# Optimization experiments

Hardware: AMD Instinct MI355X
Metric: run time of the kernel (lower is better)

The kernel has to match this reference:

```python
import jax, jax.numpy as jnp
import numpy as np
import math

B, T, D, H = 2, 2048, 1024, 16
HD = D // H  # head_dim = 64
DFF = 4 * D
EPS = 1e-5


def gelu_tanh(x):
    c = math.sqrt(2.0 / math.pi)
    return 0.5 * x * (1.0 + jnp.tanh(c * (x + 0.044715 * x ** 3)))


def layernorm(x, scale, shift):
    mean = jnp.mean(x, axis=-1, keepdims=True)
    var = jnp.mean((x - mean) ** 2, axis=-1, keepdims=True)
    return scale * (x - mean) / jnp.sqrt(var + EPS) + shift


def setup_inputs() -> dict:
    key = jax.random.key(0)
    ks = jax.random.split(key, 10)
    s_in = 1.0 / math.sqrt(D)
    s_ff = 1.0 / math.sqrt(DFF)
    return {
        "x": jax.random.normal(ks[0], (B, T, D), dtype=jnp.float32),
        "Wq": jax.random.normal(ks[1], (D, D), dtype=jnp.float32) * s_in,
        "Wk": jax.random.normal(ks[2], (D, D), dtype=jnp.float32) * s_in,
        "Wv": jax.random.normal(ks[3], (D, D), dtype=jnp.float32) * s_in,
        "Wo": jax.random.normal(ks[4], (D, D), dtype=jnp.float32) * s_in,
        "bo": jnp.zeros((D,), dtype=jnp.float32),
        "W1": jax.random.normal(ks[5], (D, DFF), dtype=jnp.float32) * s_in,
        "b1": jnp.zeros((DFF,), dtype=jnp.float32),
        "W2": jax.random.normal(ks[6], (DFF, D), dtype=jnp.float32) * s_ff,
        "b2": jnp.zeros((D,), dtype=jnp.float32),
        "g1": jnp.ones((D,), dtype=jnp.float32),
        "s1": jnp.zeros((D,), dtype=jnp.float32),
        "g2": jnp.ones((D,), dtype=jnp.float32),
        "s2": jnp.zeros((D,), dtype=jnp.float32),
    }


def reference(x, Wq, Wk, Wv, Wo, bo, W1, b1, W2, b2, g1, s1, g2, s2):
    # --- attention sublayer (pre-LN) ---
    h = layernorm(x, g1, s1)
    q = (h @ Wq).reshape(B, T, H, HD).transpose(0, 2, 1, 3)  # [B,H,T,hd]
    k = (h @ Wk).reshape(B, T, H, HD).transpose(0, 2, 1, 3)
    v = (h @ Wv).reshape(B, T, H, HD).transpose(0, 2, 1, 3)
    scores = jnp.einsum('bhqd,bhkd->bhqk', q, k) / math.sqrt(HD)
    causal = jnp.triu(jnp.ones((T, T), dtype=bool), k=1)
    scores = jnp.where(causal, -jnp.inf, scores)
    attn = jax.nn.softmax(scores, axis=-1)
    ctx = jnp.einsum('bhqk,bhkd->bhqd', attn, v)
    ctx = ctx.transpose(0, 2, 1, 3).reshape(B, T, D)
    x = x + (ctx @ Wo + bo)
    # --- feed-forward sublayer (pre-LN) ---
    h2 = layernorm(x, g2, s2)
    ff = gelu_tanh(h2 @ W1 + b1) @ W2 + b2
    return x + ff
```

## Files before the change

### kernel.cpp

```cpp
#include <hip/hip_runtime.h>
#include <cstdint>
#include <cstddef>

typedef unsigned short u16;
typedef __attribute__((ext_vector_type(8))) __bf16 bf16x8;
typedef __attribute__((ext_vector_type(8))) unsigned short u16x8;
typedef __attribute__((ext_vector_type(4))) float f32x4;
typedef __attribute__((ext_vector_type(16))) float f32x16;
typedef __attribute__((ext_vector_type(4))) unsigned short u16x4;
typedef __attribute__((ext_vector_type(2))) int i32x2;

#define DEV __device__ __forceinline__

DEV u16 f2bf(float f) {
  union { float f; unsigned u; } v; v.f = f;
  unsigned r = v.u + 0x7fffu + ((v.u >> 16) & 1u);
  return (u16)(r >> 16);
}

DEV float bf2f(u16 b) {
  unsigned u = ((unsigned)b) << 16;
  union { unsigned u; float f; } v; v.u = u;
  return v.f;
}

DEV void gload_lds16(const void* g, void* l) {
  __builtin_amdgcn_global_load_lds(
      (const __attribute__((address_space(1))) void*)g,
      (__attribute__((address_space(3))) void*)l, 16, 0, 0);
}

DEV float gelu_f(float x) {
  float u = 0.7978845608028654f * (x + 0.044715f * x * x * x);
  float t = exp2f(-2.8853900817779268f * u);
  return x * __builtin_amdgcn_rcpf(1.0f + t);
}

DEV unsigned cvtpk_bf16(float lo, float hi) {
  unsigned u;
  asm("v_cvt_pk_bf16_f32 %0, %1, %2" : "=v"(u) : "v"(lo), "v"(hi));
  return u;
}

__global__ __launch_bounds__(256) void wtrans(const float* __restrict__ W,
                                              u16* __restrict__ Wt, int K, int N) {
  __shared__ float tile[32][33];
  const int n0 = blockIdx.x * 32, k0 = blockIdx.y * 32;
  const int t = threadIdx.x, c = t & 31, r0 = t >> 5;
#pragma unroll
  for (int i = 0; i < 4; ++i) {
    int r = r0 + i * 8;
    tile[r][c] = W[(size_t)(k0 + r) * N + n0 + c];
  }
  __syncthreads();
#pragma unroll
  for (int i = 0; i < 4; ++i) {
    int r = r0 + i * 8;
    Wt[(size_t)(n0 + r) * K + k0 + c] = f2bf(tile[c][r]);
  }
}

__global__ __launch_bounds__(256) void ln_bf16(const float* __restrict__ x,
                                               const float* __restrict__ g,
                                               const float* __restrict__ s,
                                               u16* __restrict__ out) {
  const int row = blockIdx.x, t = threadIdx.x;
  const int l = t & 63, w = t >> 6;
  f32x4 v = *(const f32x4*)(x + (size_t)row * 1024 + t * 4);
  float sm = v.x + v.y + v.z + v.w;
  float s2 = v.x * v.x + v.y * v.y + v.z * v.z + v.w * v.w;
#pragma unroll
  for (int d = 1; d < 64; d <<= 1) { sm += __shfl_xor(sm, d); s2 += __shfl_xor(s2, d); }
  __shared__ float red[8];
  if (l == 0) { red[w] = sm; red[4 + w] = s2; }
  __syncthreads();
  sm = red[0] + red[1] + red[2] + red[3];
  s2 = red[4] + red[5] + red[6] + red[7];
  const float mean = sm * (1.0f / 1024.0f);
  const float rstd = rsqrtf(s2 * (1.0f / 1024.0f) - mean * mean + 1e-5f);
  f32x4 gv = *(const f32x4*)(g + t * 4);
  f32x4 sv = *(const f32x4*)(s + t * 4);
  u16x4 o;
  o.x = f2bf((v.x - mean) * rstd * gv.x + sv.x);
  o.y = f2bf((v.y - mean) * rstd * gv.y + sv.y);
  o.z = f2bf((v.z - mean) * rstd * gv.z + sv.z);
  o.w = f2bf((v.w - mean) * rstd * gv.w + sv.w);
  *(u16x4*)(out + (size_t)row * 1024 + t * 4) = o;
}

template <int EPI>
__global__ __launch_bounds__(256) void gemm_bt(const u16* __restrict__ A,
                                               const u16* __restrict__ Bt,
                                               const float* __restrict__ bias,
                                               const float* __restrict__ resid,
                                               void* __restrict__ outp,
                                               void* __restrict__ outpB,
                                               void* __restrict__ outpC,
                                               void* __restrict__ outpD,
                                               int M, int N, int K) {
  __shared__ alignas(16) u16 As[128 * 32];
  __shared__ alignas(16) u16 Bs[128 * 32];
  const int tid = threadIdx.x, l = tid & 63, w = tid >> 6;
  const int bm0 = blockIdx.x * 128, bn0 = blockIdx.y * 128;
  const int wm = (w >> 1) * 64, wn = (w & 1) * 64;
  const int lr = l & 15, lk8 = (l >> 4) * 8;

  const int z = blockIdx.z;
  const int Kc = K / gridDim.z;
  const int kbeg = z * Kc, kend = kbeg + Kc;
  void* po = outp;
  if (EPI == 3) po = (z == 0) ? outp : (z == 1) ? outpB : (z == 2) ? outpC : outpD;

  f32x4 acc[4][4];
#pragma unroll
  for (int i = 0; i < 4; ++i)
#pragma unroll
    for (int j = 0; j < 4; ++j) acc[i][j] = (f32x4){0.f, 0.f, 0.f, 0.f};

  for (int k0 = kbeg; k0 < kend; k0 += 32) {
#pragma unroll
    for (int c = 0; c < 2; ++c) {
      const int lin = c * 256 + tid;
      const int row = lin >> 2, col = (lin & 3) * 8;
      gload_lds16(A + (size_t)(bm0 + row) * K + k0 + col, (char*)As + lin * 16);
      gload_lds16(Bt + (size_t)(bn0 + row) * K + k0 + col, (char*)Bs + lin * 16);
    }
    __syncthreads();
    bf16x8 af[4], bfv[4];
#pragma unroll
    for (int i = 0; i < 4; ++i) af[i] = *(const bf16x8*)(As + (wm + i * 16 + lr) * 32 + lk8);
#pragma unroll
    for (int j = 0; j < 4; ++j) bfv[j] = *(const bf16x8*)(Bs + (wn + j * 16 + lr) * 32 + lk8);
#pragma unroll
    for (int i = 0; i < 4; ++i)
#pragma unroll
      for (int j = 0; j < 4; ++j)
        acc[i][j] = __builtin_amdgcn_mfma_f32_16x16x32_bf16(af[i], bfv[j], acc[i][j], 0, 0, 0);
    __syncthreads();
  }

#pragma unroll
  for (int i = 0; i < 4; ++i) {
#pragma unroll
    for (int r = 0; r < 4; ++r) {
      const int m = bm0 + wm + i * 16 + (l >> 4) * 4 + r;
#pragma unroll
      for (int j = 0; j < 4; ++j) {
        const int n = bn0 + wn + j * 16 + lr;
        const float va = acc[i][j][r];
        if (EPI == 0) {
          ((u16*)po)[(size_t)m * N + n] = f2bf(va);
        } else if (EPI == 1) {
          ((u16*)po)[(size_t)m * N + n] = f2bf(gelu_f(va + bias[n]));
        } else if (EPI == 2) {
          ((float*)po)[(size_t)m * N + n] = va + bias[n] + resid[(size_t)m * N + n];
        } else {
          ((u16*)po)[(size_t)m * N + n] = f2bf(va);
        }
      }
    }
  }
}

__global__ __launch_bounds__(256) void reduce4(const u16* __restrict__ p0,
                                               const u16* __restrict__ p1,
                                               const u16* __restrict__ p2,
                                               const u16* __restrict__ p3,
                                               const float* __restrict__ bias,
                                               const float* __restrict__ resid,
                                               float* __restrict__ out) {
  const int m = blockIdx.x, t = threadIdx.x;
  const size_t off = (size_t)m * 1024 + t * 4;
  const u16x4 a0 = *(const u16x4*)(p0 + off);
  const u16x4 a1 = *(const u16x4*)(p1 + off);
  const u16x4 a2 = *(const u16x4*)(p2 + off);
  const u16x4 a3 = *(const u16x4*)(p3 + off);
  const f32x4 rv = *(const f32x4*)(resid + off);
  const f32x4 bv = *(const f32x4*)(bias + t * 4);
  f32x4 o;
  o.x = bf2f(a0.x) + bf2f(a1.x) + bf2f(a2.x) + bf2f(a3.x) + bv.x + rv.x;
  o.y = bf2f(a0.y) + bf2f(a1.y) + bf2f(a2.y) + bf2f(a3.y) + bv.y + rv.y;
  o.z = bf2f(a0.z) + bf2f(a1.z) + bf2f(a2.z) + bf2f(a3.z) + bv.z + rv.z;
  o.w = bf2f(a0.w) + bf2f(a1.w) + bf2f(a2.w) + bf2f(a3.w) + bv.w + rv.w;
  *(f32x4*)(out + off) = o;
}

__global__ __launch_bounds__(256) void kvrepack(const u16* __restrict__ qkv,
                                                u16* __restrict__ Kf,
                                                u16* __restrict__ Vf) {
  const int t = blockIdx.x;
  const int bh = blockIdx.y, b = bh >> 4, h = bh & 15;
  const int tid = threadIdx.x;
  u16* kout = Kf + (size_t)bh * 131072;
  u16* vout = Vf + (size_t)bh * 131072;

#pragma unroll
  for (int i = 0; i < 2; ++i) {
    const int s = tid + i * 256;
    const int h2 = s >> 8, kc = (s >> 6) & 3, li = s & 63;
    const int lni = li & 31, hii = li >> 5;
    const u16x8 r = *(const u16x8*)(qkv +
        (size_t)(b * 2048 + t * 64 + h2 * 32 + lni) * 3072 + 1024 + h * 64 + kc * 16 + hii * 8);
    *(u16x8*)(kout + ((size_t)t * 8 + h2 * 4 + kc) * 512 + li * 8) = r;
  }

  __shared__ u16 Vt[64][72];
  {
    const int tok = tid >> 2, dc = (tid & 3) * 16;
    const u16* src = qkv + (size_t)(b * 2048 + t * 64 + tok) * 3072 + 2048 + h * 64 + dc;
    *(u16x8*)&Vt[tok][dc] = *(const u16x8*)src;
    *(u16x8*)&Vt[tok][dc + 8] = *(const u16x8*)(src + 8);
  }
  __syncthreads();
#pragma unroll
  for (int i = 0; i < 2; ++i) {
    const int s = tid + i * 256;
    const int dh = s >> 8, ks = (s >> 6) & 3, li = s & 63;
    const int lni = li & 31, hii = li >> 5;
    u16x8 o;
#pragma unroll
    for (int e = 0; e < 8; ++e) o[e] = Vt[ks * 16 + hii * 8 + e][dh * 32 + lni];
    *(u16x8*)(vout + ((size_t)t * 8 + dh * 4 + ks) * 512 + li * 8) = o;
  }
}

template <int BASE>
DEV bf16x8 pack_pfrag(const f32x16& p, int hi) {
  unsigned C = cvtpk_bf16(p[BASE + 0], p[BASE + 1]);
  unsigned D = cvtpk_bf16(p[BASE + 2], p[BASE + 3]);
  unsigned A = cvtpk_bf16(p[BASE + 4], p[BASE + 5]);
  unsigned B = cvtpk_bf16(p[BASE + 6], p[BASE + 7]);
  unsigned u0, u1, u2, u3;
#if __has_builtin(__builtin_amdgcn_permlane32_swap)
  i32x2 r02 = __builtin_amdgcn_permlane32_swap((int)C, (int)A, false, false);
  i32x2 r13 = __builtin_amdgcn_permlane32_swap((int)D, (int)B, false, false);
  u0 = (unsigned)r02.x; u2 = (unsigned)r02.y;
  u1 = (unsigned)r13.x; u3 = (unsigned)r13.y;
#else
  unsigned pC = (unsigned)__shfl_xor((int)C, 32);
  unsigned pD = (unsigned)__shfl_xor((int)D, 32);
  unsigned pA = (unsigned)__shfl_xor((int)A, 32);
  unsigned pB = (unsigned)__shfl_xor((int)B, 32);
  u0 = hi ? pA : C;  u1 = hi ? pB : D;
  u2 = hi ? A : pC;  u3 = hi ? B : pD;
#endif
  union { unsigned u[4]; bf16x8 v; } res;
  res.u[0] = u0; res.u[1] = u1; res.u[2] = u2; res.u[3] = u3;
  return res.v;
}

__global__ __launch_bounds__(64, 2) void attn_frag(const u16* __restrict__ q,
                                                   const u16* __restrict__ kf,
                                                   const u16* __restrict__ vf,
                                                   u16* __restrict__ ctx, int ldq) {
  const int qw = 63 - (int)blockIdx.x;
  const int bh = blockIdx.y, b = bh >> 4, h = bh & 15;
  const int l = (int)threadIdx.x & 63;
  const int ln = l & 31, hi = l >> 5;
  const int q0w = qw * 32;
  const int qg = q0w + ln;

  const float qscale = 0.125f * 1.44269504f;
  bf16x8 qf[4];
#pragma unroll
  for (int kc = 0; kc < 4; ++kc) {
    u16x8 raw = *(const u16x8*)(q + (size_t)(b * 2048 + qg) * ldq + h * 64 + kc * 16 + hi * 8);
    union { u16 us[8]; bf16x8 v; } sc;
#pragma unroll
    for (int e = 0; e < 8; ++e) sc.us[e] = f2bf(bf2f(raw[e]) * qscale);
    qf[kc] = sc.v;
  }

  const int nt = (qw >> 1) + 1;
  const u16* kfp = kf + (size_t)bh * 131072 + l * 8;
  const u16* vfp = vf + (size_t)bh * 131072 + l * 8;

  bf16x8 ka[4], kb[4];
#pragma unroll
  for (int kc = 0; kc < 4; ++kc) {
    ka[kc] = *(const bf16x8*)(kfp + kc * 512);
    kb[kc] = *(const bf16x8*)(kfp + 2048 + kc * 512);
  }

  f32x16 o0, o1;
#pragma unroll
  for (int r = 0; r < 16; ++r) { o0[r] = 0.f; o1[r] = 0.f; }
  float m = -1e30f, lsum = 0.f;

  for (int t = 0; t < nt; ++t) {
    const int kv0 = t * 64;
    const bool last = (t == nt - 1);
    const bool s1live = !(last && !(qw & 1));

    const u16* vb = vfp + (size_t)t * 4096;
    bf16x8 v0[4], v1[4];
#pragma unroll
    for (int ks = 0; ks < 4; ++ks) {
      v0[ks] = *(const bf16x8*)(vb + ks * 512);
      v1[ks] = *(const bf16x8*)(vb + 2048 + ks * 512);
    }

    f32x16 s0, s1;
#pragma unroll
    for (int r = 0; r < 16; ++r) { s0[r] = 0.f; s1[r] = 0.f; }
    __builtin_amdgcn_s_setprio(1);
#pragma unroll
    for (int kc = 0; kc < 4; ++kc)
      s0 = __builtin_amdgcn_mfma_f32_32x32x16_bf16(ka[kc], qf[kc], s0, 0, 0, 0);
    if (s1live) {
#pragma unroll
      for (int kc = 0; kc < 4; ++kc)
        s1 = __builtin_amdgcn_mfma_f32_32x32x16_bf16(kb[kc], qf[kc], s1, 0, 0, 0);
    }
    __builtin_amdgcn_s_setprio(0);

    {
      const u16* kn = kfp + (size_t)((t + 1 < nt) ? t + 1 : t) * 4096;
#pragma unroll
      for (int kc = 0; kc < 4; ++kc) {
        ka[kc] = *(const bf16x8*)(kn + kc * 512);
        kb[kc] = *(const bf16x8*)(kn + 2048 + kc * 512);
      }
    }

    if (last) {
#pragma unroll
      for (int r = 0; r < 16; ++r) {
        const int crow = (r & 3) + 8 * (r >> 2) + 4 * hi;
        if (qw & 1) {
          s1[r] = (kv0 + 32 + crow <= qg) ? s1[r] : -1e30f;
        } else {
          s0[r] = (kv0 + crow <= qg) ? s0[r] : -1e30f;
          s1[r] = -1e30f;
        }
      }
    }

    float pm = -1e30f;
#pragma unroll
    for (int r = 0; r < 16; ++r) pm = fmaxf(pm, fmaxf(s0[r], s1[r]));
    pm = fmaxf(pm, __shfl_xor(pm, 32));

    const float mnew = fmaxf(m, pm);
    if (!__all(pm <= m + 8.0f)) {
      const float alpha = exp2f(m - mnew);
      m = mnew;
      lsum *= alpha;
#pragma unroll
      for (int r = 0; r < 16; ++r) { o0[r] *= alpha; o1[r] *= alpha; }
    }

    float ps = 0.f;
#pragma unroll
    for (int r = 0; r < 16; ++r) {
      const float p0 = exp2f(s0[r] - m);
      const float p1 = exp2f(s1[r] - m);
      s0[r] = p0; s1[r] = p1;
      ps += p0 + p1;
    }
    ps += __shfl_xor(ps, 32);
    lsum += ps;

    bf16x8 apv[4];
    apv[0] = pack_pfrag<0>(s0, hi);
    apv[1] = pack_pfrag<8>(s0, hi);
    apv[2] = pack_pfrag<0>(s1, hi);
    apv[3] = pack_pfrag<8>(s1, hi);
    __builtin_amdgcn_s_setprio(1);
#pragma unroll
    for (int ks = 0; ks < 4; ++ks) {
      o0 = __builtin_amdgcn_mfma_f32_32x32x16_bf16(apv[ks], v0[ks], o0, 0, 0, 0);
      o1 = __builtin_amdgcn_mfma_f32_32x32x16_bf16(apv[ks], v1[ks], o1, 0, 0, 0);
    }
    __builtin_amdgcn_s_setprio(0);
  }

  const float linv = 1.0f / lsum;
#pragma unroll
  for (int r = 0; r < 16; ++r) {
    const int crow = (r & 3) + 8 * (r >> 2) + 4 * hi;
    const float lr_ = __shfl(linv, crow);
    u16* dst = ctx + (size_t)(b * 2048 + q0w + crow) * 1024 + h * 64;
    dst[ln] = f2bf(o0[r] * lr_);
    dst[32 + ln] = f2bf(o1[r] * lr_);
  }
}

extern "C" void kernel_launch(void* const* d_in, const int* in_sizes, int n_in,
                              void* d_out, int out_size, void* d_ws, size_t ws_size,
                              hipStream_t stream) {
  const float* x  = (const float*)d_in[0];
  const float* Wq = (const float*)d_in[1];
  const float* Wk = (const float*)d_in[2];
  const float* Wv = (const float*)d_in[3];
  const float* Wo = (const float*)d_in[4];
  const float* bo = (const float*)d_in[5];
  const float* W1 = (const float*)d_in[6];
  const float* b1 = (const float*)d_in[7];
  const float* W2 = (const float*)d_in[8];
  const float* b2 = (const float*)d_in[9];
  const float* g1 = (const float*)d_in[10];
  const float* s1 = (const float*)d_in[11];
  const float* g2 = (const float*)d_in[12];
  const float* s2 = (const float*)d_in[13];

  char* ws = (char*)d_ws;
  const size_t MB = 1ull << 20;
  u16*  h1    = (u16*)(ws + 0);
  u16*  wqkvT = (u16*)(ws + 8 * MB);
  u16*  woT   = (u16*)(ws + 14 * MB);
  u16*  w1T   = (u16*)(ws + 16 * MB);
  u16*  w2T   = (u16*)(ws + 24 * MB);
  u16*  qkv   = (u16*)(ws + 32 * MB);
  u16*  vfr   = (u16*)(ws + 56 * MB);
  u16*  ctx   = (u16*)(ws + 64 * MB);
  float* x2   = (float*)(ws + 72 * MB);
  u16*  ff1   = (u16*)(ws + 32 * MB);
  u16*  kfr   = h1;
  u16*  op0   = (u16*)(ws + 0);
  u16*  op1   = (u16*)(ws + 32 * MB);
  u16*  op2   = (u16*)(ws + 40 * MB);
  u16*  op3   = (u16*)(ws + 56 * MB);
  u16*  wp0   = (u16*)(ws + 0);
  u16*  wp1   = (u16*)(ws + 8 * MB);
  u16*  wp2   = (u16*)(ws + 16 * MB);
  u16*  wp3   = (u16*)(ws + 64 * MB);

  const dim3 blk(256);

  wtrans<<<dim3(32, 32),  blk, 0, stream>>>(Wq, wqkvT,                1024, 1024);
  wtrans<<<dim3(32, 32),  blk, 0, stream>>>(Wk, wqkvT + 1024 * 1024,  1024, 1024);
  wtrans<<<dim3(32, 32),  blk, 0, stream>>>(Wv, wqkvT + 2048 * 1024,  1024, 1024);
  wtrans<<<dim3(32, 32),  blk, 0, stream>>>(Wo, woT,                  1024, 1024);
  wtrans<<<dim3(128, 32), blk, 0, stream>>>(W1, w1T, 1024, 4096);
  wtrans<<<dim3(32, 128), blk, 0, stream>>>(W2, w2T, 4096, 1024);

  ln_bf16<<<dim3(4096), blk, 0, stream>>>(x, g1, s1, h1);

  gemm_bt<0><<<dim3(32, 24), blk, 0, stream>>>(h1, wqkvT, nullptr, nullptr,
                                               (void*)qkv, nullptr, nullptr, nullptr,
                                               4096, 3072, 1024);

  kvrepack<<<dim3(32, 32), blk, 0, stream>>>(qkv, kfr, vfr);

  attn_frag<<<dim3(64, 32), dim3(64), 0, stream>>>(qkv, kfr, vfr, ctx, 3072);

  gemm_bt<3><<<dim3(32, 8, 4), blk, 0, stream>>>(ctx, woT, nullptr, nullptr,
                                                 (void*)op0, (void*)op1, (void*)op2, (void*)op3,
                                                 4096, 1024, 1024);
  reduce4<<<dim3(4096), blk, 0, stream>>>(op0, op1, op2, op3, bo, x, x2);

  ln_bf16<<<dim3(4096), blk, 0, stream>>>(x2, g2, s2, h1);

  gemm_bt<1><<<dim3(32, 32), blk, 0, stream>>>(h1, w1T, b1, nullptr,
                                               (void*)ff1, nullptr, nullptr, nullptr,
                                               4096, 4096, 1024);

  gemm_bt<3><<<dim3(32, 8, 4), blk, 0, stream>>>(ff1, w2T, nullptr, nullptr,
                                                 (void*)wp0, (void*)wp1, (void*)wp2, (void*)wp3,
                                                 4096, 1024, 4096);

  reduce4<<<dim3(4096), blk, 0, stream>>>(wp0, wp1, wp2, wp3, b2, x2, (float*)d_out);
}
```

Measured before the change: 314.8 us.

## Split causal attention KV range across two blocks and merge partials

Each query tile's causal KV loop is split into two halves run by separate workgroups. Each half writes unnormalized bf16 partial outputs plus its running max and sum. A new merge kernel combines the two halves with log-sum-exp rescaling and normalizes into ctx. This doubles the grid and shortens the longest per-block loop, aiming at better occupancy and less tail imbalance from the causal triangle. The cost is an extra launch, extra partial-buffer traffic, and bf16 rounding of the unnormalized partials.

```diff
diff --git a/kernel.cpp b/kernel.cpp
--- a/kernel.cpp
+++ b/kernel.cpp
@@ -249,11 +249,14 @@
   return res.v;
 }
 
-__global__ __launch_bounds__(64, 2) void attn_frag(const u16* __restrict__ q,
-                                                   const u16* __restrict__ kf,
-                                                   const u16* __restrict__ vf,
-                                                   u16* __restrict__ ctx, int ldq) {
-  const int qw = 63 - (int)blockIdx.x;
+__global__ __launch_bounds__(64, 2) void attn_split(const u16* __restrict__ q,
+                                                    const u16* __restrict__ kf,
+                                                    const u16* __restrict__ vf,
+                                                    u16* __restrict__ opart,
+                                                    float* __restrict__ mlpart, int ldq) {
+  const int xb = blockIdx.x;
+  const int qw = 63 - (xb >> 1);
+  const int split = xb & 1;
   const int bh = blockIdx.y, b = bh >> 4, h = bh & 15;
   const int l = (int)threadIdx.x & 63;
   const int ln = l & 31, hi = l >> 5;
@@ -272,118 +275,149 @@
   }
 
   const int nt = (qw >> 1) + 1;
+  const int nt0 = nt >> 1;
+  const int tb = split ? nt0 : 0;
+  const int te = split ? nt : nt0;
+  const int dlast = nt - 1;
   const u16* kfp = kf + (size_t)bh * 131072 + l * 8;
   const u16* vfp = vf + (size_t)bh * 131072 + l * 8;
 
-  bf16x8 ka[4], kb[4];
-#pragma unroll
-  for (int kc = 0; kc < 4; ++kc) {
-    ka[kc] = *(const bf16x8*)(kfp + kc * 512);
-    kb[kc] = *(const bf16x8*)(kfp + 2048 + kc * 512);
-  }
-
   f32x16 o0, o1;
 #pragma unroll
   for (int r = 0; r < 16; ++r) { o0[r] = 0.f; o1[r] = 0.f; }
   float m = -1e30f, lsum = 0.f;
 
-  for (int t = 0; t < nt; ++t) {
-    const int kv0 = t * 64;
-    const bool last = (t == nt - 1);
-    const bool s1live = !(last && !(qw & 1));
-
-    const u16* vb = vfp + (size_t)t * 4096;
-    bf16x8 v0[4], v1[4];
-#pragma unroll
-    for (int ks = 0; ks < 4; ++ks) {
-      v0[ks] = *(const bf16x8*)(vb + ks * 512);
-      v1[ks] = *(const bf16x8*)(vb + 2048 + ks * 512);
+  if (tb < te) {
+    bf16x8 ka[4], kb[4];
+    {
+      const u16* kp = kfp + (size_t)tb * 4096;
+#pragma unroll
+      for (int kc = 0; kc < 4; ++kc) {
+        ka[kc] = *(const bf16x8*)(kp + kc * 512);
+        kb[kc] = *(const bf16x8*)(kp + 2048 + kc * 512);
+      }
     }
 
-    f32x16 s0, s1;
-#pragma unroll
-    for (int r = 0; r < 16; ++r) { s0[r] = 0.f; s1[r] = 0.f; }
-    __builtin_amdgcn_s_setprio(1);
-#pragma unroll
-    for (int kc = 0; kc < 4; ++kc)
-      s0 = __builtin_amdgcn_mfma_f32_32x32x16_bf16(ka[kc], qf[kc], s0, 0, 0, 0);
-    if (s1live) {
+    for (int t = tb; t < te; ++t) {
+      const int kv0 = t * 64;
+      const bool diag = (t == dlast);
+      const bool s1live = !(diag && !(qw & 1));
+
+      const u16* vb = vfp + (size_t)t * 4096;
+      bf16x8 v0[4], v1[4];
+#pragma unroll
+      for (int ks = 0; ks < 4; ++ks) {
+        v0[ks] = *(const bf16x8*)(vb + ks * 512);
+        v1[ks] = *(const bf16x8*)(vb + 2048 + ks * 512);
+      }
+
+      f32x16 s0, s1;
+#pragma unroll
+      for (int r = 0; r < 16; ++r) { s0[r] = 0.f; s1[r] = 0.f; }
+      __builtin_amdgcn_s_setprio(1);
 #pragma unroll
       for (int kc = 0; kc < 4; ++kc)
-        s1 = __builtin_amdgcn_mfma_f32_32x32x16_bf16(kb[kc], qf[kc], s1, 0, 0, 0);
+        s0 = __builtin_amdgcn_mfma_f32_32x32x16_bf16(ka[kc], qf[kc], s0, 0, 0, 0);
+      if (s1live) {
+#pragma unroll
+        for (int kc = 0; kc < 4; ++kc)
+          s1 = __builtin_amdgcn_mfma_f32_32x32x16_bf16(kb[kc], qf[kc], s1, 0, 0, 0);
+      }
+      __builtin_amdgcn_s_setprio(0);
+
+      {
+        const u16* kn = kfp + (size_t)((t + 1 < te) ? t + 1 : t) * 4096;
+#pragma unroll
+        for (int kc = 0; kc < 4; ++kc) {
+          ka[kc] = *(const bf16x8*)(kn + kc * 512);
+          kb[kc] = *(const bf16x8*)(kn + 2048 + kc * 512);
+        }
+      }
+
+      if (diag) {
+#pragma unroll
+        for (int r = 0; r < 16; ++r) {
+          const int crow = (r & 3) + 8 * (r >> 2) + 4 * hi;
+          if (qw & 1) {
+            s1[r] = (kv0 + 32 + crow <= qg) ? s1[r] : -1e30f;
+          } else {
+            s0[r] = (kv0 + crow <= qg) ? s0[r] : -1e30f;
+            s1[r] = -1e30f;
+          }
+        }
+      }
+
+      float pm = -1e30f;
+#pragma unroll
+      for (int r = 0; r < 16; ++r) pm = fmaxf(pm, fmaxf(s0[r], s1[r]));
+      pm = fmaxf(pm, __shfl_xor(pm, 32));
+
+      const float mnew = fmaxf(m, pm);
+      if (!__all(pm <= m + 8.0f)) {
+        const float alpha = exp2f(m - mnew);
+        m = mnew;
+        lsum *= alpha;
+#pragma unroll
+        for (int r = 0; r < 16; ++r) { o0[r] *= alpha; o1[r] *= alpha; }
+      }
+
+      float ps = 0.f;
+#pragma unroll
+      for (int r = 0; r < 16; ++r) {
+        const float p0 = exp2f(s0[r] - m);
+        const float p1 = exp2f(s1[r] - m);
+        s0[r] = p0; s1[r] = p1;
+        ps += p0 + p1;
+      }
+      ps += __shfl_xor(ps, 32);
+      lsum += ps;
+
+      bf16x8 apv[4];
+      apv[0] = pack_pfrag<0>(s0, hi);
+      apv[1] = pack_pfrag<8>(s0, hi);
+      apv[2] = pack_pfrag<0>(s1, hi);
+      apv[3] = pack_pfrag<8>(s1, hi);
+      __builtin_amdgcn_s_setprio(1);
+#pragma unroll
+      for (int ks = 0; ks < 4; ++ks) {
+        o0 = __builtin_amdgcn_mfma_f32_32x32x16_bf16(apv[ks], v0[ks], o0, 0, 0, 0);
+        o1 = __builtin_amdgcn_mfma_f32_32x32x16_bf16(apv[ks], v1[ks], o1, 0, 0, 0);
+      }
+      __builtin_amdgcn_s_setprio(0);
     }
-    __builtin_amdgcn_s_setprio(0);
-
-    {
-      const u16* kn = kfp + (size_t)((t + 1 < nt) ? t + 1 : t) * 4096;
-#pragma unroll
-      for (int kc = 0; kc < 4; ++kc) {
-        ka[kc] = *(const bf16x8*)(kn + kc * 512);
-        kb[kc] = *(const bf16x8*)(kn + 2048 + kc * 512);
-      }
-    }
-
-    if (last) {
-#pragma unroll
-      for (int r = 0; r < 16; ++r) {
-        const int crow = (r & 3) + 8 * (r >> 2) + 4 * hi;
-        if (qw & 1) {
-          s1[r] = (kv0 + 32 + crow <= qg) ? s1[r] : -1e30f;
-        } else {
-          s0[r] = (kv0 + crow <= qg) ? s0[r] : -1e30f;
-          s1[r] = -1e30f;
-        }
-      }
-    }
-
-    float pm = -1e30f;
-#pragma unroll
-    for (int r = 0; r < 16; ++r) pm = fmaxf(pm, fmaxf(s0[r], s1[r]));
-    pm = fmaxf(pm, __shfl_xor(pm, 32));
-
-    const float mnew = fmaxf(m, pm);
-    if (!__all(pm <= m + 8.0f)) {
-      const float alpha = exp2f(m - mnew);
-      m = mnew;
-      lsum *= alpha;
-#pragma unroll
-      for (int r = 0; r < 16; ++r) { o0[r] *= alpha; o1[r] *= alpha; }
-    }
-
-    float ps = 0.f;
-#pragma unroll
-    for (int r = 0; r < 16; ++r) {
-      const float p0 = exp2f(s0[r] - m);
-      const float p1 = exp2f(s1[r] - m);
-      s0[r] = p0; s1[r] = p1;
-      ps += p0 + p1;
-    }
-    ps += __shfl_xor(ps, 32);
-    lsum += ps;
-
-    bf16x8 apv[4];
-    apv[0] = pack_pfrag<0>(s0, hi);
-    apv[1] = pack_pfrag<8>(s0, hi);
-    apv[2] = pack_pfrag<0>(s1, hi);
-    apv[3] = pack_pfrag<8>(s1, hi);
-    __builtin_amdgcn_s_setprio(1);
-#pragma unroll
-    for (int ks = 0; ks < 4; ++ks) {
-      o0 = __builtin_amdgcn_mfma_f32_32x32x16_bf16(apv[ks], v0[ks], o0, 0, 0, 0);
-      o1 = __builtin_amdgcn_mfma_f32_32x32x16_bf16(apv[ks], v1[ks], o1, 0, 0, 0);
-    }
-    __builtin_amdgcn_s_setprio(0);
-  }
-
-  const float linv = 1.0f / lsum;
+  }
+
+  u16* ob = opart + ((size_t)xb * 32 + bh) * 2048;
+  float* mlb = mlpart + ((size_t)xb * 32 + bh) * 64;
 #pragma unroll
   for (int r = 0; r < 16; ++r) {
     const int crow = (r & 3) + 8 * (r >> 2) + 4 * hi;
-    const float lr_ = __shfl(linv, crow);
-    u16* dst = ctx + (size_t)(b * 2048 + q0w + crow) * 1024 + h * 64;
-    dst[ln] = f2bf(o0[r] * lr_);
-    dst[32 + ln] = f2bf(o1[r] * lr_);
-  }
+    ob[crow * 64 + ln] = f2bf(o0[r]);
+    ob[crow * 64 + 32 + ln] = f2bf(o1[r]);
+  }
+  if (hi == 0) mlb[ln] = m; else mlb[32 + ln] = lsum;
+}
+
+__global__ __launch_bounds__(256) void attn_merge(const u16* __restrict__ opart,
+                                                  const float* __restrict__ mlpart,
+                                                  u16* __restrict__ ctx) {
+  const int qw = blockIdx.x, bh = blockIdx.y, b = bh >> 4, h = bh & 15;
+  const int tid = threadIdx.x;
+  const int q = tid >> 3, dg = (tid & 7) * 8;
+  const size_t base0 = (size_t)((63 - qw) * 2) * 32 + bh;
+  const size_t base1 = base0 + 32;
+  const float m0 = mlpart[base0 * 64 + q], l0 = mlpart[base0 * 64 + 32 + q];
+  const float m1 = mlpart[base1 * 64 + q], l1 = mlpart[base1 * 64 + 32 + q];
+  const float mn = fmaxf(m0, m1);
+  const float f0 = exp2f(m0 - mn), f1 = exp2f(m1 - mn);
+  const float linv = 1.0f / (f0 * l0 + f1 * l1);
+  const u16x8 a = *(const u16x8*)(opart + base0 * 2048 + q * 64 + dg);
+  const u16x8 c = *(const u16x8*)(opart + base1 * 2048 + q * 64 + dg);
+  u16x8 o;
+#pragma unroll
+  for (int e = 0; e < 8; ++e)
+    o[e] = f2bf((f0 * bf2f(a[e]) + f1 * bf2f(c[e])) * linv);
+  *(u16x8*)(ctx + (size_t)(b * 2048 + qw * 32 + q) * 1024 + h * 64 + dg) = o;
 }
 
 extern "C" void kernel_launch(void* const* d_in, const int* in_sizes, int n_in,
@@ -417,6 +451,8 @@
   float* x2   = (float*)(ws + 72 * MB);
   u16*  ff1   = (u16*)(ws + 32 * MB);
   u16*  kfr   = h1;
+  u16*   opart  = (u16*)(ws + 72 * MB);
+  float* mlpart = (float*)(ws + 8 * MB);
   u16*  op0   = (u16*)(ws + 0);
   u16*  op1   = (u16*)(ws + 32 * MB);
   u16*  op2   = (u16*)(ws + 40 * MB);
@@ -443,7 +479,8 @@
 
   kvrepack<<<dim3(32, 32), blk, 0, stream>>>(qkv, kfr, vfr);
 
-  attn_frag<<<dim3(64, 32), dim3(64), 0, stream>>>(qkv, kfr, vfr, ctx, 3072);
+  attn_split<<<dim3(128, 32), dim3(64), 0, stream>>>(qkv, kfr, vfr, opart, mlpart, 3072);
+  attn_merge<<<dim3(64, 32), blk, 0, stream>>>(opart, mlpart, ctx);
 
   gemm_bt<3><<<dim3(32, 8, 4), blk, 0, stream>>>(ctx, woT, nullptr, nullptr,
                                                  (void*)op0, (void*)op1, (void*)op2, (void*)op3,
```

New measurement: 310.6 us. Within noise of the previous version (-1.3%).
